# Optimization experiments

Hardware: AMD Instinct MI355X
Metric: run time of the kernel (lower is better)

## Reference

```python
import jax, jax.numpy as jnp
import numpy as np

B, T, D = 2, 2048, 1024
N_HEADS, D_HEAD, WINDOW = 16, 64, 256
SCALE = D_HEAD ** -0.5


def setup_inputs() -> dict:
    key = jax.random.key(0)
    k1, k2, k3 = jax.random.split(key, 3)
    x = jax.random.normal(k1, (B, T, D), dtype=jnp.float32)
    # torch Linear weights are [out_features, in_features], init std=0.02
    w_qkv = jax.random.normal(k2, (3 * N_HEADS * D_HEAD, D), dtype=jnp.float32) * 0.02
    w_out = jax.random.normal(k3, (D, N_HEADS * D_HEAD), dtype=jnp.float32) * 0.02
    return {"x": x, "w_qkv": w_qkv, "w_out": w_out}


def reference(x, w_qkv, w_out):
    b, t, d = x.shape
    qkv = jnp.einsum('btd,ed->bte', x, w_qkv)  # [B,T,3*H*Dh]
    q, k, v = jnp.split(qkv, 3, axis=-1)
    def heads(u):
        return u.reshape(b, t, N_HEADS, D_HEAD).transpose(0, 2, 1, 3)  # [B,H,T,Dh]
    q, k, v = heads(q), heads(k), heads(v)
    scores = jnp.einsum('bhqd,bhkd->bhqk', q, k) * SCALE  # [B,H,T,T]
    pos = jnp.arange(t)
    dist = pos[:, None] - pos[None, :]  # query - key
    allowed = (dist >= 0) & (dist < WINDOW)  # causal sliding window
    neg_inf = jnp.asarray(-jnp.inf, dtype=scores.dtype)
    scores = jnp.where(allowed[None, None], scores, neg_inf)
    attn = jax.nn.softmax(scores, axis=-1)
    out = jnp.einsum('bhqk,bhkd->bhqd', attn, v)  # [B,H,T,Dh]
    out = out.transpose(0, 2, 1, 3).reshape(b, t, N_HEADS * D_HEAD)
    return jnp.einsum('bte,de->btd', out, w_out)
```

## Files before the change

### kernel.cpp

```cpp
#include <hip/hip_runtime.h>
#include <hip/hip_bf16.h>

typedef unsigned short bfu;
typedef __attribute__((ext_vector_type(8))) short short8;
typedef __attribute__((ext_vector_type(4))) float floatx4;

#define B_ 2
#define T_ 2048
#define D_ 1024
#define NH 16
#define DH 64
#define WIN 256
#define QKV_COLS 3072

__device__ __forceinline__ bfu f2b_bits(float f) {
  union { __hip_bfloat16 h; bfu u; } cv;
  cv.h = __float2bfloat16(f);
  return cv.u;
}

__global__ void cvt_f2b_kernel(const float* __restrict__ in, bfu* __restrict__ out, int n) {
  int i = (blockIdx.x * 256 + threadIdx.x) * 4;
  if (i >= n) return;
  floatx4 v = *(const floatx4*)(in + i);
  out[i + 0] = f2b_bits(v.x);
  out[i + 1] = f2b_bits(v.y);
  out[i + 2] = f2b_bits(v.z);
  out[i + 3] = f2b_bits(v.w);
}

template <bool OUT_BF16>
__global__ __launch_bounds__(256) void gemm_bt_kernel(const bfu* __restrict__ A,
                                                      const bfu* __restrict__ Bm,
                                                      void* __restrict__ C,
                                                      int M, int N, int K) {
  __shared__ __align__(16) bfu As[128][72];
  __shared__ __align__(16) bfu Bs[128][72];
  const int tid = threadIdx.x;
  const int wave = tid >> 6, lane = tid & 63;
  const int quad = lane >> 4, cl = lane & 15;
  const int wm = (wave >> 1) * 64, wn = (wave & 1) * 64;
  const int m0 = blockIdx.y * 128, n0 = blockIdx.x * 128;

  floatx4 acc[4][4] = {};

  for (int k0 = 0; k0 < K; k0 += 64) {
    __syncthreads();
#pragma unroll
    for (int i = 0; i < 4; ++i) {
      int c = tid + i * 256;
      int row = c >> 3, col = (c & 7) * 8;
      *(short8*)(&As[row][col]) = *(const short8*)(A + (size_t)(m0 + row) * K + (k0 + col));
      *(short8*)(&Bs[row][col]) = *(const short8*)(Bm + (size_t)(n0 + row) * K + (k0 + col));
    }
    __syncthreads();
#pragma unroll
    for (int ks = 0; ks < 2; ++ks) {
      const int kq = ks * 32 + quad * 8;
      short8 af[4], bfr[4];
#pragma unroll
      for (int im = 0; im < 4; ++im) af[im] = *(const short8*)(&As[wm + im * 16 + cl][kq]);
#pragma unroll
      for (int in = 0; in < 4; ++in) bfr[in] = *(const short8*)(&Bs[wn + in * 16 + cl][kq]);
#pragma unroll
      for (int im = 0; im < 4; ++im)
#pragma unroll
        for (int in = 0; in < 4; ++in)
          acc[im][in] = __builtin_amdgcn_mfma_f32_16x16x32_bf16(af[im], bfr[in], acc[im][in], 0, 0, 0);
    }
  }
#pragma unroll
  for (int im = 0; im < 4; ++im) {
#pragma unroll
    for (int r = 0; r < 4; ++r) {
      const size_t row = (size_t)(m0 + wm + im * 16 + quad * 4 + r);
#pragma unroll
      for (int in = 0; in < 4; ++in) {
        const size_t idx = row * (size_t)N + (n0 + wn + in * 16 + cl);
        if constexpr (OUT_BF16)
          ((bfu*)C)[idx] = f2b_bits(acc[im][in][r]);
        else
          ((float*)C)[idx] = acc[im][in][r];
      }
    }
  }
}

__global__ __launch_bounds__(256) void swa_kernel(const bfu* __restrict__ qkv,
                                                  bfu* __restrict__ aout) {
  __shared__ __align__(16) bfu Qs[64][72];
  __shared__ __align__(16) bfu Ks[64][72];
  __shared__ __align__(16) bfu Vt[64][72];
  __shared__ __align__(16) bfu Ps[4][16][72];

  const int qt = blockIdx.x, h = blockIdx.y, b = blockIdx.z;
  const int tid = threadIdx.x, wave = tid >> 6, lane = tid & 63;
  const int quad = lane >> 4, cl = lane & 15;
  const int q0 = qt * 64;
  const bfu* qb = qkv + (size_t)b * T_ * QKV_COLS + h * DH;
  const bfu* kb = qb + 1024;
  const bfu* vb = qb + 2048;

#pragma unroll
  for (int i = 0; i < 2; ++i) {
    int c = tid + i * 256;
    int row = c >> 3, col = (c & 7) * 8;
    *(short8*)(&Qs[row][col]) = *(const short8*)(qb + (size_t)(q0 + row) * QKV_COLS + col);
  }

  float m_r[4], l_r[4];
  floatx4 acc_o[4] = {};
#pragma unroll
  for (int r = 0; r < 4; ++r) { m_r[r] = -1e30f; l_r[r] = 0.f; }

  const int jt0 = (qt >= 4) ? qt - 4 : 0;
  for (int jt = jt0; jt <= qt; ++jt) {
    const int k0 = jt * 64;
    __syncthreads();
#pragma unroll
    for (int i = 0; i < 2; ++i) {
      int c = tid + i * 256;
      int row = c >> 3, col = (c & 7) * 8;
      *(short8*)(&Ks[row][col]) = *(const short8*)(kb + (size_t)(k0 + row) * QKV_COLS + col);
      union { short8 v; bfu u[8]; } tmp;
      tmp.v = *(const short8*)(vb + (size_t)(k0 + row) * QKV_COLS + col);
#pragma unroll
      for (int e = 0; e < 8; ++e) Vt[col + e][row] = tmp.u[e];
    }
    __syncthreads();

    floatx4 s[4] = {};
#pragma unroll
    for (int ks = 0; ks < 2; ++ks) {
      const int kq = ks * 32 + quad * 8;
      short8 aq = *(const short8*)(&Qs[wave * 16 + cl][kq]);
#pragma unroll
      for (int j = 0; j < 4; ++j) {
        short8 bk = *(const short8*)(&Ks[j * 16 + cl][kq]);
        s[j] = __builtin_amdgcn_mfma_f32_16x16x32_bf16(aq, bk, s[j], 0, 0, 0);
      }
    }

#pragma unroll
    for (int r = 0; r < 4; ++r) {
      const int qg = q0 + wave * 16 + quad * 4 + r;
      float mx = -1e30f;
#pragma unroll
      for (int j = 0; j < 4; ++j) {
        const int kg = k0 + j * 16 + cl;
        const int dist = qg - kg;
        const float v = (dist >= 0 && dist < WIN) ? s[j][r] * 0.125f : -1e30f;
        s[j][r] = v;
        mx = fmaxf(mx, v);
      }
      mx = fmaxf(mx, __shfl_xor(mx, 1));
      mx = fmaxf(mx, __shfl_xor(mx, 2));
      mx = fmaxf(mx, __shfl_xor(mx, 4));
      mx = fmaxf(mx, __shfl_xor(mx, 8));
      const float mn = fmaxf(m_r[r], mx);
      const float alpha = __expf(m_r[r] - mn);
      m_r[r] = mn;
      float ssum = 0.f;
#pragma unroll
      for (int j = 0; j < 4; ++j) {
        const float p = (s[j][r] <= -1e29f) ? 0.f : __expf(s[j][r] - mn);
        s[j][r] = p;
        ssum += p;
      }
      l_r[r] = l_r[r] * alpha + ssum;
#pragma unroll
      for (int j = 0; j < 4; ++j) acc_o[j][r] *= alpha;
    }

#pragma unroll
    for (int j = 0; j < 4; ++j)
#pragma unroll
      for (int r = 0; r < 4; ++r)
        Ps[wave][quad * 4 + r][j * 16 + cl] = f2b_bits(s[j][r]);
#pragma unroll
    for (int ks = 0; ks < 2; ++ks) {
      const int kq = ks * 32 + quad * 8;
      short8 ap = *(const short8*)(&Ps[wave][cl][kq]);
#pragma unroll
      for (int j = 0; j < 4; ++j) {
        short8 bv = *(const short8*)(&Vt[j * 16 + cl][kq]);
        acc_o[j] = __builtin_amdgcn_mfma_f32_16x16x32_bf16(ap, bv, acc_o[j], 0, 0, 0);
      }
    }
  }

#pragma unroll
  for (int r = 0; r < 4; ++r) {
    float l = l_r[r];
    l += __shfl_xor(l, 1);
    l += __shfl_xor(l, 2);
    l += __shfl_xor(l, 4);
    l += __shfl_xor(l, 8);
    l_r[r] = 1.f / l;
  }
  bfu* ob = aout + (size_t)b * T_ * D_ + h * DH;
#pragma unroll
  for (int r = 0; r < 4; ++r) {
    const size_t row = (size_t)(q0 + wave * 16 + quad * 4 + r);
#pragma unroll
    for (int j = 0; j < 4; ++j)
      ob[row * D_ + j * 16 + cl] = f2b_bits(acc_o[j][r] * l_r[r]);
  }
}

extern "C" void kernel_launch(void* const* d_in, const int* in_sizes, int n_in,
                              void* d_out, int out_size, void* d_ws, size_t ws_size,
                              hipStream_t stream) {
  const float* x     = (const float*)d_in[0];
  const float* w_qkv = (const float*)d_in[1];
  const float* w_out = (const float*)d_in[2];
  float* out = (float*)d_out;
  char* ws = (char*)d_ws;

  bfu* xb    = (bfu*)(ws);
  bfu* wqkvb = (bfu*)(ws + (8ull << 20));
  bfu* woutb = (bfu*)(ws + (14ull << 20));
  bfu* qkvb  = (bfu*)(ws + (16ull << 20));
  bfu* attb  = (bfu*)(ws + (40ull << 20));

  const int nx  = B_ * T_ * D_;
  const int nwq = QKV_COLS * D_;
  const int nwo = D_ * NH * DH;

  cvt_f2b_kernel<<<nx / 1024, 256, 0, stream>>>(x, xb, nx);
  cvt_f2b_kernel<<<nwq / 1024, 256, 0, stream>>>(w_qkv, wqkvb, nwq);
  cvt_f2b_kernel<<<nwo / 1024, 256, 0, stream>>>(w_out, woutb, nwo);

  gemm_bt_kernel<true><<<dim3(QKV_COLS / 128, (B_ * T_) / 128), 256, 0, stream>>>(
      xb, wqkvb, qkvb, B_ * T_, QKV_COLS, D_);

  swa_kernel<<<dim3(T_ / 64, NH, B_), 256, 0, stream>>>(qkvb, attb);

  gemm_bt_kernel<false><<<dim3(D_ / 128, (B_ * T_) / 128), 256, 0, stream>>>(
      attb, woutb, out, B_ * T_, D_, D_);
}
```

Baseline: 175.1 us.

## Use direct global-to-LDS loads with XOR swizzle, fuse conversions, narrow output GEMM tile

The GEMM and attention tile loads now use global_load_lds (direct global-to-LDS DMA) into unpadded tiles with an XOR swizzle, which avoids the register round trip while keeping LDS reads free of bank conflicts. The V transpose store uses a matching swizzle. The three fp32-to-bf16 conversion launches become one kernel that relies on the workspace buffers being contiguous. The output projection GEMM uses 64-wide N tiles so it launches twice as many blocks for better CU occupancy. The swizzle indexing and the layout assumptions of the LDS DMA path are the main correctness risks.

```diff
diff --git a/kernel.cpp b/kernel.cpp
--- a/kernel.cpp
+++ b/kernel.cpp
@@ -12,6 +12,9 @@
 #define DH 64
 #define WIN 256
 #define QKV_COLS 3072
+#define NX  (B_ * T_ * D_)
+#define NWQ (QKV_COLS * D_)
+#define NWO (D_ * D_)
 
 __device__ __forceinline__ bfu f2b_bits(float f) {
   union { __hip_bfloat16 h; bfu u; } cv;
@@ -19,53 +22,71 @@
   return cv.u;
 }
 
-__global__ void cvt_f2b_kernel(const float* __restrict__ in, bfu* __restrict__ out, int n) {
+__device__ __forceinline__ void gl_lds16(const bfu* g, bfu* l) {
+  __builtin_amdgcn_global_load_lds(
+      (const __attribute__((address_space(1))) unsigned int*)g,
+      (__attribute__((address_space(3))) unsigned int*)l, 16, 0, 0);
+}
+
+__global__ void cvt3_kernel(const float* __restrict__ x, const float* __restrict__ wq,
+                            const float* __restrict__ wo, bfu* __restrict__ out) {
   int i = (blockIdx.x * 256 + threadIdx.x) * 4;
-  if (i >= n) return;
-  floatx4 v = *(const floatx4*)(in + i);
+  const float* src;
+  int off;
+  if (i < NX)            { src = x;  off = 0; }
+  else if (i < NX + NWQ) { src = wq; off = NX; }
+  else                   { src = wo; off = NX + NWQ; }
+  floatx4 v = *(const floatx4*)(src + (i - off));
   out[i + 0] = f2b_bits(v.x);
   out[i + 1] = f2b_bits(v.y);
   out[i + 2] = f2b_bits(v.z);
   out[i + 3] = f2b_bits(v.w);
 }
 
-template <bool OUT_BF16>
+template <bool OUT_BF16, int TN>
 __global__ __launch_bounds__(256) void gemm_bt_kernel(const bfu* __restrict__ A,
                                                       const bfu* __restrict__ Bm,
                                                       void* __restrict__ C,
                                                       int M, int N, int K) {
-  __shared__ __align__(16) bfu As[128][72];
-  __shared__ __align__(16) bfu Bs[128][72];
+  constexpr int NJ = TN / 32;
+  __shared__ __align__(16) bfu As[128][64];
+  __shared__ __align__(16) bfu Bs[TN][64];
   const int tid = threadIdx.x;
   const int wave = tid >> 6, lane = tid & 63;
   const int quad = lane >> 4, cl = lane & 15;
-  const int wm = (wave >> 1) * 64, wn = (wave & 1) * 64;
-  const int m0 = blockIdx.y * 128, n0 = blockIdx.x * 128;
-
-  floatx4 acc[4][4] = {};
+  const int lr = lane >> 3, lg = lane & 7, sg = lg ^ lr;
+  const int wm = (wave >> 1) * 64, wn = (wave & 1) * (TN / 2);
+  const int m0 = blockIdx.y * 128, n0 = blockIdx.x * TN;
+
+  floatx4 acc[4][NJ] = {};
 
   for (int k0 = 0; k0 < K; k0 += 64) {
     __syncthreads();
 #pragma unroll
     for (int i = 0; i < 4; ++i) {
-      int c = tid + i * 256;
-      int row = c >> 3, col = (c & 7) * 8;
-      *(short8*)(&As[row][col]) = *(const short8*)(A + (size_t)(m0 + row) * K + (k0 + col));
-      *(short8*)(&Bs[row][col]) = *(const short8*)(Bm + (size_t)(n0 + row) * K + (k0 + col));
+      const int row = i * 32 + wave * 8;
+      gl_lds16(A + (size_t)(m0 + row + lr) * K + k0 + sg * 8, &As[row][0]);
+    }
+#pragma unroll
+    for (int i = 0; i < TN / 32; ++i) {
+      const int row = i * 32 + wave * 8;
+      gl_lds16(Bm + (size_t)(n0 + row + lr) * K + k0 + sg * 8, &Bs[row][0]);
     }
     __syncthreads();
 #pragma unroll
     for (int ks = 0; ks < 2; ++ks) {
-      const int kq = ks * 32 + quad * 8;
-      short8 af[4], bfr[4];
-#pragma unroll
-      for (int im = 0; im < 4; ++im) af[im] = *(const short8*)(&As[wm + im * 16 + cl][kq]);
-#pragma unroll
-      for (int in = 0; in < 4; ++in) bfr[in] = *(const short8*)(&Bs[wn + in * 16 + cl][kq]);
+      const int gsw = ks * 4 + quad;
+      short8 af[4], bfr[NJ];
 #pragma unroll
       for (int im = 0; im < 4; ++im)
-#pragma unroll
-        for (int in = 0; in < 4; ++in)
+        af[im] = *(const short8*)(&As[wm + im * 16 + cl][(gsw ^ (cl & 7)) << 3]);
+#pragma unroll
+      for (int in = 0; in < NJ; ++in)
+        bfr[in] = *(const short8*)(&Bs[wn + in * 16 + cl][(gsw ^ (cl & 7)) << 3]);
+#pragma unroll
+      for (int im = 0; im < 4; ++im)
+#pragma unroll
+        for (int in = 0; in < NJ; ++in)
           acc[im][in] = __builtin_amdgcn_mfma_f32_16x16x32_bf16(af[im], bfr[in], acc[im][in], 0, 0, 0);
     }
   }
@@ -75,7 +96,7 @@
     for (int r = 0; r < 4; ++r) {
       const size_t row = (size_t)(m0 + wm + im * 16 + quad * 4 + r);
 #pragma unroll
-      for (int in = 0; in < 4; ++in) {
+      for (int in = 0; in < NJ; ++in) {
         const size_t idx = row * (size_t)N + (n0 + wn + in * 16 + cl);
         if constexpr (OUT_BF16)
           ((bfu*)C)[idx] = f2b_bits(acc[im][in][r]);
@@ -88,14 +109,15 @@
 
 __global__ __launch_bounds__(256) void swa_kernel(const bfu* __restrict__ qkv,
                                                   bfu* __restrict__ aout) {
-  __shared__ __align__(16) bfu Qs[64][72];
-  __shared__ __align__(16) bfu Ks[64][72];
-  __shared__ __align__(16) bfu Vt[64][72];
+  __shared__ __align__(16) bfu Qs[64][64];
+  __shared__ __align__(16) bfu Ks[64][64];
+  __shared__ __align__(16) bfu Vs[64][64];
   __shared__ __align__(16) bfu Ps[4][16][72];
 
   const int qt = blockIdx.x, h = blockIdx.y, b = blockIdx.z;
   const int tid = threadIdx.x, wave = tid >> 6, lane = tid & 63;
   const int quad = lane >> 4, cl = lane & 15;
+  const int lr = lane >> 3, lg = lane & 7, sg = lg ^ lr;
   const int q0 = qt * 64;
   const bfu* qb = qkv + (size_t)b * T_ * QKV_COLS + h * DH;
   const bfu* kb = qb + 1024;
@@ -103,9 +125,8 @@
 
 #pragma unroll
   for (int i = 0; i < 2; ++i) {
-    int c = tid + i * 256;
-    int row = c >> 3, col = (c & 7) * 8;
-    *(short8*)(&Qs[row][col]) = *(const short8*)(qb + (size_t)(q0 + row) * QKV_COLS + col);
+    const int row = wave * 16 + i * 8;
+    gl_lds16(qb + (size_t)(q0 + row + lr) * QKV_COLS + sg * 8, &Qs[row][0]);
   }
 
   float m_r[4], l_r[4];
@@ -119,24 +140,32 @@
     __syncthreads();
 #pragma unroll
     for (int i = 0; i < 2; ++i) {
-      int c = tid + i * 256;
-      int row = c >> 3, col = (c & 7) * 8;
-      *(short8*)(&Ks[row][col]) = *(const short8*)(kb + (size_t)(k0 + row) * QKV_COLS + col);
+      const int row = wave * 16 + i * 8;
+      gl_lds16(kb + (size_t)(k0 + row + lr) * QKV_COLS + sg * 8, &Ks[row][0]);
+    }
+#pragma unroll
+    for (int i = 0; i < 2; ++i) {
+      const int c = tid + i * 256;
+      const int row = c >> 3, col = (c & 7) * 8;
       union { short8 v; bfu u[8]; } tmp;
       tmp.v = *(const short8*)(vb + (size_t)(k0 + row) * QKV_COLS + col);
 #pragma unroll
-      for (int e = 0; e < 8; ++e) Vt[col + e][row] = tmp.u[e];
+      for (int e = 0; e < 8; ++e) {
+        const int d = col + e;
+        const int swz = (d & 7) ^ ((d >> 3) & 7);
+        Vs[d][((((row >> 3) ^ swz) & 7) << 3) | (row & 7)] = tmp.u[e];
+      }
     }
     __syncthreads();
 
     floatx4 s[4] = {};
 #pragma unroll
     for (int ks = 0; ks < 2; ++ks) {
-      const int kq = ks * 32 + quad * 8;
-      short8 aq = *(const short8*)(&Qs[wave * 16 + cl][kq]);
-#pragma unroll
-      for (int j = 0; j < 4; ++j) {
-        short8 bk = *(const short8*)(&Ks[j * 16 + cl][kq]);
+      const int gsw = ks * 4 + quad;
+      short8 aq = *(const short8*)(&Qs[wave * 16 + cl][(gsw ^ (cl & 7)) << 3]);
+#pragma unroll
+      for (int j = 0; j < 4; ++j) {
+        short8 bk = *(const short8*)(&Ks[j * 16 + cl][(gsw ^ (cl & 7)) << 3]);
         s[j] = __builtin_amdgcn_mfma_f32_16x16x32_bf16(aq, bk, s[j], 0, 0, 0);
       }
     }
@@ -183,7 +212,9 @@
       short8 ap = *(const short8*)(&Ps[wave][cl][kq]);
 #pragma unroll
       for (int j = 0; j < 4; ++j) {
-        short8 bv = *(const short8*)(&Vt[j * 16 + cl][kq]);
+        const int d = j * 16 + cl;
+        const int swz = (d & 7) ^ ((d >> 3) & 7);
+        short8 bv = *(const short8*)(&Vs[d][(((ks * 4 + quad) ^ swz) & 7) << 3]);
         acc_o[j] = __builtin_amdgcn_mfma_f32_16x16x32_bf16(ap, bv, acc_o[j], 0, 0, 0);
       }
     }
@@ -223,19 +254,13 @@
   bfu* qkvb  = (bfu*)(ws + (16ull << 20));
   bfu* attb  = (bfu*)(ws + (40ull << 20));
 
-  const int nx  = B_ * T_ * D_;
-  const int nwq = QKV_COLS * D_;
-  const int nwo = D_ * NH * DH;
-
-  cvt_f2b_kernel<<<nx / 1024, 256, 0, stream>>>(x, xb, nx);
-  cvt_f2b_kernel<<<nwq / 1024, 256, 0, stream>>>(w_qkv, wqkvb, nwq);
-  cvt_f2b_kernel<<<nwo / 1024, 256, 0, stream>>>(w_out, woutb, nwo);
-
-  gemm_bt_kernel<true><<<dim3(QKV_COLS / 128, (B_ * T_) / 128), 256, 0, stream>>>(
+  cvt3_kernel<<<(NX + NWQ + NWO) / 1024, 256, 0, stream>>>(x, w_qkv, w_out, xb);
+
+  gemm_bt_kernel<true, 128><<<dim3(QKV_COLS / 128, (B_ * T_) / 128), 256, 0, stream>>>(
       xb, wqkvb, qkvb, B_ * T_, QKV_COLS, D_);
 
   swa_kernel<<<dim3(T_ / 64, NH, B_), 256, 0, stream>>>(qkvb, attb);
 
-  gemm_bt_kernel<false><<<dim3(D_ / 128, (B_ * T_) / 128), 256, 0, stream>>>(
+  gemm_bt_kernel<false, 64><<<dim3(D_ / 64, (B_ * T_) / 128), 256, 0, stream>>>(
       attb, woutb, out, B_ * T_, D_, D_);
 }
```

Measured after the change: 156.2 us. 1.12x faster.
